# Kernel tuning notes

Measured on AMD Instinct MI355X. Metric: run time of the kernel, lower is better.

Reference implementation:

```python
import jax, jax.numpy as jnp
from jax import lax
import numpy as np

UNITS = 256
H = W = 64
INPUT_DIM = 128
FLAT = 64 * (H - 3) * (W - 3)  # conv stack output after same-conv, valid-conv, 2x2 avgpool stride 1


def setup_inputs() -> dict:
    key = jax.random.key(0)
    ks = jax.random.split(key, 8)
    s = lambda k, shape, fan: jax.random.normal(k, shape, jnp.float32) / np.sqrt(fan)
    return {
        "inputs": jax.random.normal(ks[0], (1, INPUT_DIM), jnp.float32),
        "memory": jax.random.normal(ks[1], (H * W, UNITS), jnp.float32),
        "conv_kernel1": s(ks[2], (3, 3, UNITS, 32), 9 * UNITS),
        "conv_kernel2": s(ks[3], (3, 3, 32, 64), 9 * 32),
        "conv_dense1": s(ks[4], (FLAT, 128), FLAT),
        "conv_dense2": s(ks[5], (128, UNITS), 128),
        "context_kernel": s(ks[6], (INPUT_DIM + UNITS, UNITS), INPUT_DIM + UNITS),
        "recurr_kernel": s(ks[7], (INPUT_DIM + UNITS, UNITS), UNITS),
        "x": 32,
        "y": 17,
    }


def reference(inputs, memory, conv_kernel1, conv_kernel2, conv_dense1,
              conv_dense2, context_kernel, recurrent_kernel=None, recurr_kernel=None,
              x=32, y=17):
    rec = recurr_kernel if recurr_kernel is not None else recurrent_kernel
    input_dim = inputs.shape[-1]
    # memory: (H*W, units) -> (1, units, H, W)  (channels_first)
    mem = memory.T.reshape(1, UNITS, H, W)
    dn = ("NCHW", "HWIO", "NCHW")
    c1 = lax.conv_general_dilated(mem, conv_kernel1, (1, 1), "SAME", dimension_numbers=dn)   # (1,32,H,W)
    c2 = lax.conv_general_dilated(c1, conv_kernel2, (1, 1), "VALID", dimension_numbers=dn)   # (1,64,H-2,W-2)
    pool = lax.reduce_window(c2, 0.0, lax.add, (1, 1, 2, 2), (1, 1, 1, 1), "VALID") * 0.25   # (1,64,H-3,W-3)
    flat = pool.reshape(1, -1)
    r_t = (flat @ conv_dense1) @ conv_dense2                      # (1, units)
    q_t = jnp.concatenate([inputs, r_t], axis=-1) @ context_kernel  # (1, units)
    m = mem[0]                                                    # (units, H, W)
    m2 = m.reshape(UNITS, H * W)
    scores = q_t @ m2                                             # (1, H*W)
    at = jax.nn.softmax(scores, axis=-1)                          # softmax over all positions
    c_t = at @ m2.T                                               # (1, units) attention read
    write_kernel = rec[:input_dim]
    write_update = rec[input_dim:]
    s_t = inputs @ write_kernel                                   # (1, units)
    global_imp = jnp.sum(s_t * r_t)
    local_imp = jnp.sum(s_t * c_t)
    mem_t = m[:, x, y][None, :]                                   # gather single slot (1, units)
    mem_t = mem_t + local_imp / (local_imp + global_imp) * ((mem_t - s_t) @ write_update)
    new_mem = m.at[:, x, y].set(mem_t[0])                         # scatter slot back
    return c_t, r_t, new_mem
```

## Files before the change

### kernel.cpp

```cpp
#include <hip/hip_runtime.h>

#define FLAT  238144
#define NB_R1 931

#define W_C2   0
#define W_P1   246016
#define W_RT   365184
#define W_ST   365440
#define W_QT   365696
#define W_QTA  365952
#define W_STAT 366208
#define W_PC   366336
#define W_WARM 382720
#define W_C1P  382736
#define W_END  1431312

#define F_C2   140416
#define F_P1   386432
#define F_RT   505600
#define F_ST   505856
#define F_QT   506112
#define F_QTA  506368
#define F_STAT 510464
#define F_PC   510592

__device__ __forceinline__ int read_idx(const int* p) {
    unsigned int u = (unsigned int)*p;
    int ex = (int)((u >> 23) & 0xFF);
    int v;
    if (ex >= 118 && ex <= 140) {
        union { unsigned int i; float f; } c; c.i = u;
        v = (int)(c.f + 0.5f);
    } else {
        v = (int)u;
    }
    return v < 0 ? 0 : (v > 63 ? 63 : v);
}

__global__ __launch_bounds__(256) void k_front(const float* __restrict__ mem,
                                               const float* __restrict__ k1,
                                               float* __restrict__ c1p,
                                               const int* __restrict__ px,
                                               const int* __restrict__ py,
                                               float* __restrict__ outm,
                                               const float* __restrict__ inp,
                                               const float* __restrict__ rec,
                                               const float* __restrict__ ck,
                                               const float* __restrict__ d2,
                                               float* __restrict__ st,
                                               float* __restrict__ qta,
                                               float* __restrict__ warm,
                                               int mode) {
    __shared__ __align__(16) float SM[12576];
    int t = threadIdx.x;
    int bid = blockIdx.x;
    if (mode == 1 && bid >= 512) {
        if (bid < 768) {
            int tu = bid - 512;
            float* tile = SM;
            int p0 = (tu & 63) * 64;
            int u0 = (tu >> 6) * 64;
            int x = read_idx(px), y = read_idx(py);
            int pxy = x * 64 + y;
            int lane = t & 63, grp = t >> 6;
            for (int r = 0; r < 16; ++r) {
                int pr = grp + r * 4;
                tile[pr * 65 + lane] = mem[(size_t)(p0 + pr) * 256 + u0 + lane];
            }
            __syncthreads();
            for (int r = 0; r < 16; ++r) {
                int ur = grp + r * 4;
                if (p0 + lane != pxy)
                    outm[(size_t)(u0 + ur) * 4096 + p0 + lane] =
                        tile[lane * 65 + ur];
            }
        } else if (bid == 768) {
            float sv = 0.f;
            #pragma unroll 16
            for (int k = 0; k < 128; ++k) sv += inp[k] * rec[k * 256 + t];
            st[t] = sv;
        } else if (bid == 769) {
            float q = 0.f;
            #pragma unroll 16
            for (int k = 0; k < 128; ++k) q += inp[k] * ck[k * 256 + t];
            qta[t] = q;
        } else {
            int wu = bid - 770;
            float a = 0.f;
            for (int k = 0; k < 12; ++k) {
                int j = (wu * 256 + t) + k * 3584;
                if (j < 40960) {
                    float4 v;
                    if (j < 8192)        v = ((const float4*)d2 )[j];
                    else if (j < 24576)  v = ((const float4*)rec)[j];
                    else                 v = ((const float4*)ck )[j - 16384];
                    a += v.x + v.y + v.z + v.w;
                }
            }
            SM[t] = a;
            __syncthreads();
            if (t == 0) {
                float s = 0.f;
                for (int i = 0; i < 256; ++i) s += SM[i];
                warm[wu] = s;
            }
        }
        return;
    }
    float* sm = SM;
    float* sk = SM + 3360;
    int th = ((bid & 63) >> 3) * 8;
    int tw = (bid & 7) * 8;
    int chunk = bid >> 6;
    {
        float4 mv[4];
        #pragma unroll
        for (int k = 0; k < 4; ++k) {
            int u = t + k * 256;
            float4 v = make_float4(0.f, 0.f, 0.f, 0.f);
            if (u < 800) {
                int pix = u >> 3, c4 = u & 7;
                int hh = th - 1 + pix / 10;
                int ww = tw - 1 + pix % 10;
                if ((unsigned)hh < 64u && (unsigned)ww < 64u)
                    v = *(const float4*)(mem + (size_t)(hh * 64 + ww) * 256
                                             + chunk * 32 + c4 * 4);
            }
            mv[k] = v;
        }
        #pragma unroll
        for (int k = 0; k < 4; ++k) {
            int u = t + k * 256;
            if (u < 800) {
                int pix = u >> 3, c4 = u & 7;
                int ib = c4 * 4;
                sm[(ib    ) * 105 + pix] = mv[k].x;
                sm[(ib + 1) * 105 + pix] = mv[k].y;
                sm[(ib + 2) * 105 + pix] = mv[k].z;
                sm[(ib + 3) * 105 + pix] = mv[k].w;
            }
        }
    }
    {
        float4 kv[9];
        #pragma unroll
        for (int k = 0; k < 9; ++k)
            kv[k] = ((const float4*)(k1 + (size_t)k * 8192
                                        + (size_t)chunk * 1024))[t];
        #pragma unroll
        for (int k = 0; k < 9; ++k)
            *(float4*)&sk[k * 1024 + t * 4] = kv[k];
    }
    __syncthreads();
    int lh = (t & 63) >> 3, lw = t & 7, og = t >> 6;
    float acc[8];
    #pragma unroll
    for (int j = 0; j < 8; ++j) acc[j] = 0.f;
    for (int dh = 0; dh < 3; ++dh)
        for (int dw = 0; dw < 3; ++dw) {
            int pixb = (lh + dh) * 10 + (lw + dw);
            const float* kt = sk + (dh * 3 + dw) * 1024 + og * 8;
            #pragma unroll 4
            for (int i = 0; i < 32; ++i) {
                float m = sm[i * 105 + pixb];
                float4 ka = *(const float4*)(kt + i * 32);
                float4 kb = *(const float4*)(kt + i * 32 + 4);
                acc[0] += m * ka.x; acc[1] += m * ka.y;
                acc[2] += m * ka.z; acc[3] += m * ka.w;
                acc[4] += m * kb.x; acc[5] += m * kb.y;
                acc[6] += m * kb.z; acc[7] += m * kb.w;
            }
        }
    int p = (th + lh) * 64 + tw + lw;
    float* dst = c1p + (size_t)chunk * 131072 + (size_t)(og * 8) * 4096 + p;
    #pragma unroll
    for (int j = 0; j < 8; ++j)
        dst[(size_t)j * 4096] = acc[j];
}

__global__ __launch_bounds__(256) void k_c1red(float* __restrict__ c1p) {
    int idx = blockIdx.x * 256 + threadIdx.x;
    float s = 0.f;
    #pragma unroll
    for (int c = 0; c < 8; ++c) s += c1p[(size_t)c * 131072 + idx];
    c1p[idx] = s;
}

__global__ __launch_bounds__(256) void k_conv2(const float* __restrict__ c1p,
                                               const float* __restrict__ k2,
                                               float* __restrict__ c2,
                                               int nchunks) {
    __shared__ float sm[32 * 104];
    __shared__ __align__(16) float sk2[9 * 32 * 16];
    int t = threadIdx.x;
    int th = (blockIdx.x >> 3) * 8;
    int tw = (blockIdx.x & 7) * 8;
    int o0 = blockIdx.y * 16;
    if (nchunks == 8) {
        #pragma unroll 2
        for (int u = t; u < 3200; u += 256) {
            int i = u / 100;
            int pix = u % 100;
            int hh = th + pix / 10;
            int ww = tw + pix % 10;
            float v = 0.f;
            if (hh < 64 && ww < 64) {
                const float* p = c1p + (size_t)i * 4096 + hh * 64 + ww;
                float a0 = p[0];
                float a1 = p[131072];
                float a2 = p[2 * 131072];
                float a3 = p[3 * 131072];
                float a4 = p[4 * 131072];
                float a5 = p[5 * 131072];
                float a6 = p[6 * 131072];
                float a7 = p[7 * 131072];
                v = a0 + a1 + a2 + a3 + a4 + a5 + a6 + a7;
            }
            sm[i * 104 + pix] = v;
        }
    } else {
        for (int u = t; u < 3200; u += 256) {
            int i = u / 100;
            int pix = u % 100;
            int hh = th + pix / 10;
            int ww = tw + pix % 10;
            float v = 0.f;
            if (hh < 64 && ww < 64)
                v = c1p[(size_t)i * 4096 + hh * 64 + ww];
            sm[i * 104 + pix] = v;
        }
    }
    {
        float4 kv[5];
        #pragma unroll
        for (int k = 0; k < 5; ++k) {
            int u = t + k * 256;
            if (u < 1152) {
                int tap = u >> 7, r = u & 127;
                int i = r >> 2, o4 = r & 3;
                kv[k] = *(const float4*)(k2 + (size_t)tap * 2048 + i * 64
                                            + o0 + o4 * 4);
            }
        }
        #pragma unroll
        for (int k = 0; k < 5; ++k) {
            int u = t + k * 256;
            if (u < 1152) {
                int tap = u >> 7, r = u & 127;
                int i = r >> 2, o4 = r & 3;
                *(float4*)&sk2[tap * 512 + i * 16 + o4 * 4] = kv[k];
            }
        }
    }
    __syncthreads();
    int pix = t & 63;
    int lh = pix >> 3, lw = pix & 7, og = t >> 6;
    float acc[4] = {0.f, 0.f, 0.f, 0.f};
    for (int dh = 0; dh < 3; ++dh)
        for (int dw = 0; dw < 3; ++dw) {
            int pixb = (lh + dh) * 10 + (lw + dw);
            const float* kt = sk2 + (dh * 3 + dw) * 512 + og * 4;
            #pragma unroll 8
            for (int i = 0; i < 32; ++i) {
                float m = sm[i * 104 + pixb];
                float4 kv = *(const float4*)(kt + i * 16);
                acc[0] += m * kv.x; acc[1] += m * kv.y;
                acc[2] += m * kv.z; acc[3] += m * kv.w;
            }
        }
    int h = th + lh, w = tw + lw;
    if (h < 62 && w < 62) {
        #pragma unroll
        for (int j = 0; j < 4; ++j)
            c2[(size_t)(o0 + og * 4 + j) * 3844 + h * 62 + w] = acc[j];
    }
}

__global__ __launch_bounds__(256) void k_r1p(const float* __restrict__ c2,
                                             const float* __restrict__ d1,
                                             float* __restrict__ p1) {
    __shared__ __align__(16) float SM[4160];
    int t = threadIdx.x;
    int fb = blockIdx.x;
    float* pl   = SM;
    float* sred = SM + 256;
    int f0 = fb * 256;
    int fmax = FLAT - f0; if (fmax > 256) fmax = 256;
    for (int s = t; s < fmax; s += 256) {
        int f = f0 + s;
        int o = f / 3721;
        int r = f % 3721;
        int h = r / 61, w = r % 61;
        const float* b = c2 + (size_t)o * 3844 + h * 62 + w;
        pl[s] = 0.25f * (b[0] + b[1] + b[62] + b[63]);
    }
    __syncthreads();
    int jq = t & 31, g = t >> 5;
    float4 a = make_float4(0.f, 0.f, 0.f, 0.f);
    if (fmax == 256) {
        #pragma unroll 16
        for (int it = 0; it < 32; ++it) {
            int s = g + it * 8;
            float m = pl[s];
            float4 dv = *(const float4*)(d1 + (size_t)(f0 + s) * 128 + jq * 4);
            a.x += m * dv.x; a.y += m * dv.y; a.z += m * dv.z; a.w += m * dv.w;
        }
    } else {
        for (int s = g; s < fmax; s += 8) {
            float m = pl[s];
            float4 dv = *(const float4*)(d1 + (size_t)(f0 + s) * 128 + jq * 4);
            a.x += m * dv.x; a.y += m * dv.y; a.z += m * dv.z; a.w += m * dv.w;
        }
    }
    *(float4*)&sred[(g * 32 + jq) * 4] = a;
    __syncthreads();
    if (t < 32) {
        float4 s4 = make_float4(0.f, 0.f, 0.f, 0.f);
        #pragma unroll
        for (int gg = 0; gg < 8; ++gg) {
            float4 v = *(const float4*)&sred[(gg * 32 + t) * 4];
            s4.x += v.x; s4.y += v.y; s4.z += v.z; s4.w += v.w;
        }
        *(float4*)(p1 + (size_t)fb * 128 + t * 4) = s4;
    }
}

__global__ __launch_bounds__(1024) void k_fused(const float* __restrict__ p1,
                                                const float* __restrict__ d2,
                                                const float* __restrict__ inp,
                                                const float* __restrict__ ck,
                                                const float* __restrict__ rec,
                                                const float* __restrict__ qta,
                                                float* __restrict__ rt,
                                                float* __restrict__ qt,
                                                float* __restrict__ st,
                                                int haveAux) {
    __shared__ float p2s[8][128];
    __shared__ float s_r1[128], s_in[128], s_rt[256];
    int t = threadIdx.x;
    int j = t & 127, part = t >> 7;
    int b0 = part * 117;
    int b1 = b0 + 117; if (b1 > NB_R1) b1 = NB_R1;
    float s = 0.f;
    #pragma unroll 8
    for (int b = b0; b < b1; ++b) s += p1[b * 128 + j];
    p2s[part][j] = s;
    if (t < 128) s_in[t] = inp[t];
    __syncthreads();
    if (t < 128) {
        float r = 0.f;
        #pragma unroll
        for (int c = 0; c < 8; ++c) r += p2s[c][t];
        s_r1[t] = r;
    }
    __syncthreads();
    if (t < 256) {
        float a = 0.f;
        #pragma unroll 16
        for (int k = 0; k < 128; ++k) a += s_r1[k] * d2[k * 256 + t];
        rt[t] = a; s_rt[t] = a;
        if (!haveAux) {
            float sv = 0.f;
            #pragma unroll 16
            for (int k = 0; k < 128; ++k) sv += s_in[k] * rec[k * 256 + t];
            st[t] = sv;
        }
    }
    __syncthreads();
    if (t < 256) {
        float q;
        if (haveAux) {
            q = qta[t];
        } else {
            q = 0.f;
            #pragma unroll 16
            for (int k = 0; k < 128; ++k) q += s_in[k] * ck[k * 256 + t];
        }
        #pragma unroll 16
        for (int k = 0; k < 256; ++k) q += s_rt[k] * ck[(128 + k) * 256 + t];
        qt[t] = q;
    }
}

__global__ __launch_bounds__(256) void k_scores(const float* __restrict__ qt,
                                                const float* __restrict__ mem,
                                                float* __restrict__ stat,
                                                float* __restrict__ pc) {
    __shared__ float q[256];
    __shared__ float rowv[64], aL[64];
    __shared__ float mbS;
    int t = threadIdx.x;
    int bid = blockIdx.x;
    q[t] = qt[t];
    __syncthreads();
    int wave = t >> 6, lane = t & 63;
    float qx = q[lane * 4], qy = q[lane * 4 + 1],
          qz = q[lane * 4 + 2], qw = q[lane * 4 + 3];
    int p0 = bid * 64;
    for (int r = 0; r < 16; ++r) {
        int p = p0 + wave * 16 + r;
        float4 m = *(const float4*)(mem + (size_t)p * 256 + lane * 4);
        float acc = m.x * qx + m.y * qy + m.z * qz + m.w * qw;
        for (int off = 32; off; off >>= 1) acc += __shfl_down(acc, off);
        if (lane == 0) rowv[wave * 16 + r] = acc;
    }
    __syncthreads();
    if (t == 0) {
        float mb = rowv[0];
        for (int i = 1; i < 64; ++i) mb = fmaxf(mb, rowv[i]);
        mbS = mb;
    }
    __syncthreads();
    if (t < 64) aL[t] = expf(rowv[t] - mbS);
    __syncthreads();
    if (t == 0) {
        float sb = 0.f;
        for (int i = 0; i < 64; ++i) sb += aL[i];
        stat[bid * 2]     = mbS;
        stat[bid * 2 + 1] = sb;
    }
    float acc = 0.f;
    #pragma unroll 16
    for (int pp = 0; pp < 64; ++pp)
        acc += aL[pp] * mem[(size_t)(p0 + pp) * 256 + t];
    pc[bid * 256 + t] = acc;
}

__global__ __launch_bounds__(256) void k_final(const float* __restrict__ rt,
                                               const float* __restrict__ st,
                                               const float* __restrict__ stat,
                                               const float* __restrict__ pc,
                                               const float* __restrict__ mem,
                                               const float* __restrict__ rec,
                                               const int* __restrict__ px,
                                               const int* __restrict__ py,
                                               float* __restrict__ out) {
    __shared__ float s_diff[256], red[256];
    __shared__ float sm_[64], wb[64], aux[2];
    int t = threadIdx.x;
    int x = read_idx(px), y = read_idx(py);
    int pxy = x * 64 + y;
    if (t < 64) sm_[t] = stat[t * 2];
    __syncthreads();
    if (t == 0) {
        float M = sm_[0];
        for (int i = 1; i < 64; ++i) M = fmaxf(M, sm_[i]);
        float S = 0.f;
        for (int i = 0; i < 64; ++i) S += stat[i * 2 + 1] * expf(sm_[i] - M);
        aux[0] = M; aux[1] = 1.f / S;
    }
    __syncthreads();
    if (t < 64) wb[t] = expf(sm_[t] - aux[0]) * aux[1];
    __syncthreads();
    float ctv = 0.f;
    #pragma unroll 16
    for (int b = 0; b < 64; ++b) ctv += pc[b * 256 + t] * wb[b];
    float stv = st[t], rtv = rt[t];
    float memt = mem[(size_t)pxy * 256 + t];
    red[t] = stv * rtv; __syncthreads();
    for (int s = 128; s; s >>= 1) { if (t < s) red[t] += red[t + s]; __syncthreads(); }
    float gimp = red[0]; __syncthreads();
    red[t] = stv * ctv; __syncthreads();
    for (int s = 128; s; s >>= 1) { if (t < s) red[t] += red[t + s]; __syncthreads(); }
    float limp = red[0];
    s_diff[t] = memt - stv;
    __syncthreads();
    float d = 0.f;
    #pragma unroll 16
    for (int k = 0; k < 256; ++k)
        d += s_diff[k] * rec[(128 + k) * 256 + t];
    float frac = limp / (limp + gimp);
    out[t] = ctv;
    out[256 + t] = rtv;
    out[512 + (size_t)t * 4096 + pxy] = memt + frac * d;
}

__global__ __launch_bounds__(256) void k_transpose(const float* __restrict__ mem,
                                                   const int* __restrict__ px,
                                                   const int* __restrict__ py,
                                                   float* __restrict__ outm) {
    __shared__ float tile[64][65];
    int t = threadIdx.x;
    int p0 = blockIdx.x * 64;
    int u0 = blockIdx.y * 64;
    int x = read_idx(px), y = read_idx(py);
    int pxy = x * 64 + y;
    int lane = t & 63, grp = t >> 6;
    for (int r = 0; r < 16; ++r) {
        int pr = grp + r * 4;
        tile[pr][lane] = mem[(size_t)(p0 + pr) * 256 + u0 + lane];
    }
    __syncthreads();
    for (int r = 0; r < 16; ++r) {
        int ur = grp + r * 4;
        if (p0 + lane != pxy)
            outm[(size_t)(u0 + ur) * 4096 + p0 + lane] = tile[lane][ur];
    }
}

extern "C" void kernel_launch(void* const* d_in, const int* in_sizes, int n_in,
                              void* d_out, int out_size, void* d_ws, size_t ws_size,
                              hipStream_t stream) {
    const float* inp = (const float*)d_in[0];
    const float* mem = (const float*)d_in[1];
    const float* k1  = (const float*)d_in[2];
    const float* k2  = (const float*)d_in[3];
    const float* d1  = (const float*)d_in[4];
    const float* d2  = (const float*)d_in[5];
    const float* ck  = (const float*)d_in[6];
    const float* rec = (const float*)d_in[7];
    const int* px = (const int*)d_in[8];
    const int* py = (const int*)d_in[9];
    float* out = (float*)d_out;
    float* scr = out + 512;
    float* ws  = (float*)d_ws;

    bool useWs = (ws != nullptr) && (ws_size >= (size_t)W_END * sizeof(float));

    if (useWs) {
        k_front<<<784, 256, 0, stream>>>(mem, k1, ws + W_C1P, px, py, scr,
                                         inp, rec, ck, d2,
                                         ws + W_ST, ws + W_QTA, ws + W_WARM, 1);
        k_conv2<<<dim3(64, 4), 256, 0, stream>>>(ws + W_C1P, k2, ws + W_C2, 8);
        k_r1p<<<NB_R1, 256, 0, stream>>>(ws + W_C2, d1, ws + W_P1);
        k_fused<<<1, 1024, 0, stream>>>(ws + W_P1, d2, inp, ck, rec,
                                        ws + W_QTA, ws + W_RT, ws + W_QT,
                                        ws + W_ST, 1);
        k_scores<<<64, 256, 0, stream>>>(ws + W_QT, mem, ws + W_STAT,
                                         ws + W_PC);
        k_final<<<1, 256, 0, stream>>>(ws + W_RT, ws + W_ST, ws + W_STAT,
                                       ws + W_PC, mem, rec, px, py, out);
    } else {
        k_front<<<512, 256, 0, stream>>>(mem, k1, scr, px, py, scr,
                                         inp, rec, ck, d2,
                                         scr + F_ST, scr + F_QTA,
                                         scr + F_PC + 16384, 0);
        k_c1red<<<512, 256, 0, stream>>>(scr);
        k_conv2<<<dim3(64, 4), 256, 0, stream>>>(scr, k2, scr + F_C2, 1);
        k_r1p<<<NB_R1, 256, 0, stream>>>(scr + F_C2, d1, scr + F_P1);
        k_fused<<<1, 1024, 0, stream>>>(scr + F_P1, d2, inp, ck, rec,
                                        scr + F_QTA, scr + F_RT, scr + F_QT,
                                        scr + F_ST, 0);
        k_scores<<<64, 256, 0, stream>>>(scr + F_QT, mem, scr + F_STAT,
                                         scr + F_PC);
        k_final<<<1, 256, 0, stream>>>(scr + F_RT, scr + F_ST, scr + F_STAT,
                                       scr + F_PC, mem, rec, px, py, out);
        k_transpose<<<dim3(64, 4), 256, 0, stream>>>(mem, px, py, out + 512);
    }
}
```

Baseline: 278.0 us.

## Prefetch dense1 weights and precompute write-update during conv2 using extra blocks

Adds extra blocks to the conv2 launch. Most of them stream the large conv_dense1 weight matrix into a dummy sink so it is resident in cache when the dense-reduction kernel runs. One of them computes the (mem_t - s_t) @ write_update matvec early, so the single-block final kernel only reads the result. The goal is to overlap HBM traffic with conv2 compute and shorten the serial tail, at the risk of stealing bandwidth from conv2 and of the cache not retaining the prefetched data.

```diff
diff --git a/kernel.cpp b/kernel.cpp
--- a/kernel.cpp
+++ b/kernel.cpp
@@ -12,8 +12,10 @@
 #define W_STAT 366208
 #define W_PC   366336
 #define W_WARM 382720
-#define W_C1P  382736
-#define W_END  1431312
+#define W_D    382736
+#define W_SINK 382992
+#define W_C1P  383120
+#define W_END  1431696
 
 #define F_C2   140416
 #define F_P1   386432
@@ -189,10 +191,58 @@
 __global__ __launch_bounds__(256) void k_conv2(const float* __restrict__ c1p,
                                                const float* __restrict__ k2,
                                                float* __restrict__ c2,
-                                               int nchunks) {
-    __shared__ float sm[32 * 104];
+                                               int nchunks,
+                                               const float* __restrict__ d1,
+                                               const float* __restrict__ mem,
+                                               const float* __restrict__ st,
+                                               const float* __restrict__ rec,
+                                               const int* __restrict__ px,
+                                               const int* __restrict__ py,
+                                               float* __restrict__ dout,
+                                               float* __restrict__ sink) {
+    __shared__ __align__(16) float smu[32 * 104 > 512 ? 32 * 104 : 512];
     __shared__ __align__(16) float sk2[9 * 32 * 16];
     int t = threadIdx.x;
+    if (blockIdx.y >= 4) {
+        if (blockIdx.y == 4 && blockIdx.x == 0) {
+            float* s_diff = smu;
+            int x = read_idx(px), y = read_idx(py);
+            int pxy = x * 64 + y;
+            s_diff[t] = mem[(size_t)pxy * 256 + t] - st[t];
+            __syncthreads();
+            float d = 0.f;
+            #pragma unroll 16
+            for (int k = 0; k < 256; ++k)
+                d += s_diff[k] * rec[(128 + k) * 256 + t];
+            dout[t] = d;
+        } else {
+            int pb = (blockIdx.y - 4) * 64 + blockIdx.x - 1;
+            const float4* dp = (const float4*)d1;
+            float a = 0.f;
+            #pragma unroll
+            for (int rr = 0; rr < 12; ++rr) {
+                float4 v[8];
+                #pragma unroll
+                for (int k = 0; k < 8; ++k) {
+                    size_t j = (size_t)(pb * 256 + t)
+                             + (size_t)(rr * 8 + k) * 32512;
+                    v[k] = dp[j];
+                }
+                #pragma unroll
+                for (int k = 0; k < 8; ++k)
+                    a += v[k].x + v[k].y + v[k].z + v[k].w;
+            }
+            smu[t] = a;
+            __syncthreads();
+            if (t == 0) {
+                float s = 0.f;
+                for (int i = 0; i < 256; ++i) s += smu[i];
+                sink[pb] = s;
+            }
+        }
+        return;
+    }
+    float* sm = smu;
     int th = (blockIdx.x >> 3) * 8;
     int tw = (blockIdx.x & 7) * 8;
     int o0 = blockIdx.y * 16;
@@ -434,7 +484,9 @@
                                                const float* __restrict__ rec,
                                                const int* __restrict__ px,
                                                const int* __restrict__ py,
-                                               float* __restrict__ out) {
+                                               const float* __restrict__ dpre,
+                                               float* __restrict__ out,
+                                               int haveD) {
     __shared__ float s_diff[256], red[256];
     __shared__ float sm_[64], wb[64], aux[2];
     int t = threadIdx.x;
@@ -463,12 +515,17 @@
     red[t] = stv * ctv; __syncthreads();
     for (int s = 128; s; s >>= 1) { if (t < s) red[t] += red[t + s]; __syncthreads(); }
     float limp = red[0];
-    s_diff[t] = memt - stv;
-    __syncthreads();
-    float d = 0.f;
-    #pragma unroll 16
-    for (int k = 0; k < 256; ++k)
-        d += s_diff[k] * rec[(128 + k) * 256 + t];
+    float d;
+    if (haveD) {
+        d = dpre[t];
+    } else {
+        s_diff[t] = memt - stv;
+        __syncthreads();
+        d = 0.f;
+        #pragma unroll 16
+        for (int k = 0; k < 256; ++k)
+            d += s_diff[k] * rec[(128 + k) * 256 + t];
+    }
     float frac = limp / (limp + gimp);
     out[t] = ctv;
     out[256 + t] = rtv;
@@ -521,7 +578,9 @@
         k_front<<<784, 256, 0, stream>>>(mem, k1, ws + W_C1P, px, py, scr,
                                          inp, rec, ck, d2,
                                          ws + W_ST, ws + W_QTA, ws + W_WARM, 1);
-        k_conv2<<<dim3(64, 4), 256, 0, stream>>>(ws + W_C1P, k2, ws + W_C2, 8);
+        k_conv2<<<dim3(64, 6), 256, 0, stream>>>(ws + W_C1P, k2, ws + W_C2, 8,
+                                                 d1, mem, ws + W_ST, rec,
+                                                 px, py, ws + W_D, ws + W_SINK);
         k_r1p<<<NB_R1, 256, 0, stream>>>(ws + W_C2, d1, ws + W_P1);
         k_fused<<<1, 1024, 0, stream>>>(ws + W_P1, d2, inp, ck, rec,
                                         ws + W_QTA, ws + W_RT, ws + W_QT,
@@ -529,14 +588,18 @@
         k_scores<<<64, 256, 0, stream>>>(ws + W_QT, mem, ws + W_STAT,
                                          ws + W_PC);
         k_final<<<1, 256, 0, stream>>>(ws + W_RT, ws + W_ST, ws + W_STAT,
-                                       ws + W_PC, mem, rec, px, py, out);
+                                       ws + W_PC, mem, rec, px, py,
+                                       ws + W_D, out, 1);
     } else {
         k_front<<<512, 256, 0, stream>>>(mem, k1, scr, px, py, scr,
                                          inp, rec, ck, d2,
                                          scr + F_ST, scr + F_QTA,
                                          scr + F_PC + 16384, 0);
         k_c1red<<<512, 256, 0, stream>>>(scr);
-        k_conv2<<<dim3(64, 4), 256, 0, stream>>>(scr, k2, scr + F_C2, 1);
+        k_conv2<<<dim3(64, 4), 256, 0, stream>>>(scr, k2, scr + F_C2, 1,
+                                                 d1, mem, scr + F_ST, rec,
+                                                 px, py, scr + F_PC + 16400,
+                                                 scr + F_PC + 16656);
         k_r1p<<<NB_R1, 256, 0, stream>>>(scr + F_C2, d1, scr + F_P1);
         k_fused<<<1, 1024, 0, stream>>>(scr + F_P1, d2, inp, ck, rec,
                                         scr + F_QTA, scr + F_RT, scr + F_QT,
@@ -544,7 +607,8 @@
         k_scores<<<64, 256, 0, stream>>>(scr + F_QT, mem, scr + F_STAT,
                                          scr + F_PC);
         k_final<<<1, 256, 0, stream>>>(scr + F_RT, scr + F_ST, scr + F_STAT,
-                                       scr + F_PC, mem, rec, px, py, out);
+                                       scr + F_PC, mem, rec, px, py,
+                                       scr, out, 0);
         k_transpose<<<dim3(64, 4), 256, 0, stream>>>(mem, px, py, out + 512);
     }
 }
```

Measured after the change: 272.7 us. No clear change (-1.9%).
